# Performance work log

Measured on AMD Instinct MI355X. Metric: run time of the kernel, lower is better.

## Reference

```python
import jax, jax.numpy as jnp
import numpy as np

N, IN_DIM, HID, HEADS, OUT = 4096, 512, 256, 2, 40
LN_EPS = 1e-5


def setup_inputs() -> dict:
    key = jax.random.key(0)
    ks = jax.random.split(key, 12)
    s_in = 1.0 / np.sqrt(IN_DIM)
    s_o = 1.0 / np.sqrt(2 * HID)
    adj = jax.random.randint(ks[0], (HEADS, N, N), 0, 2).astype(jnp.float32)
    h = jax.random.normal(ks[1], (N, IN_DIM), dtype=jnp.float32)
    Wq = jax.random.uniform(ks[2], (HEADS, IN_DIM, HID), minval=-s_in, maxval=s_in)
    bq = jax.random.uniform(ks[3], (HEADS, HID), minval=-s_in, maxval=s_in)
    Wk = jax.random.uniform(ks[4], (HEADS, IN_DIM, HID), minval=-s_in, maxval=s_in)
    bk = jax.random.uniform(ks[5], (HEADS, HID), minval=-s_in, maxval=s_in)
    Wv = jax.random.uniform(ks[6], (HEADS, IN_DIM, HID), minval=-s_in, maxval=s_in)
    bv = jax.random.uniform(ks[7], (HEADS, HID), minval=-s_in, maxval=s_in)
    Wo = jax.random.uniform(ks[8], (2 * HID, IN_DIM), minval=-s_o, maxval=s_o)
    bo = jax.random.uniform(ks[9], (IN_DIM,), minval=-s_o, maxval=s_o)
    gamma = jnp.ones((IN_DIM,), jnp.float32)
    beta = jnp.zeros((IN_DIM,), jnp.float32)
    Wp = jax.random.uniform(ks[10], (IN_DIM, OUT), minval=-s_in, maxval=s_in)
    bp = jax.random.uniform(ks[11], (OUT,), minval=-s_in, maxval=s_in)
    return dict(adj=adj, h=h, Wq=Wq, bq=bq, Wk=Wk, bk=bk, Wv=Wv, bv=bv,
                Wo=Wo, bo=bo, gamma=gamma, beta=beta, Wp=Wp, bp=bp)


def reference(adj, h, Wq, bq, Wk, bk, Wv, bv, Wo, bo, gamma, beta, Wp, bp):
    # Per-head projections, vectorized over the head axis. [H, N, D]
    Q = jnp.einsum('ni,hid->hnd', h, Wq) + bq[:, None, :]
    K = jnp.einsum('ni,hid->hnd', h, Wk) + bk[:, None, :]
    V = jnp.einsum('ni,hid->hnd', h, Wv) + bv[:, None, :]
    # Dense QK^T, elementwise-multiplied (not -inf masked) by per-head adjacency.
    scores = jnp.einsum('hnd,hmd->hnm', Q, K) * adj          # [H, N, N]
    attn = jax.nn.softmax(scores, axis=-1)
    X = jnp.einsum('hnm,hmd->hnd', attn, V)                  # [H, N, D]
    # cat([X0, X1], dim=1) -> [N, H*D]
    X_final = jnp.transpose(X, (1, 0, 2)).reshape(N, HEADS * HID)
    z = X_final @ Wo + bo                                    # [N, IN_DIM]
    mu = jnp.mean(z, axis=-1, keepdims=True)
    var = jnp.var(z, axis=-1, keepdims=True)
    M = (z - mu) * jax.lax.rsqrt(var + LN_EPS) * gamma + beta
    return jax.nn.softmax(M @ Wp + bp, axis=1)               # [N, OUT]
```

## Files before the change

### kernel.cpp

```cpp
#include <hip/hip_runtime.h>
#include <hip/hip_bf16.h>

#define N_TOK 4096
#define D_IN  512
#define D_HID 256
#define N_OUT 40

typedef _Float16 half8 __attribute__((ext_vector_type(8)));
typedef _Float16 half4 __attribute__((ext_vector_type(4)));
typedef float    f32x4 __attribute__((ext_vector_type(4)));

__device__ __forceinline__ void async_copy16(const _Float16* g, _Float16* l) {
  __builtin_amdgcn_global_load_lds(
      (const __attribute__((address_space(1))) unsigned int*)(g),
      (__attribute__((address_space(3))) unsigned int*)(l), 16, 0, 0);
}

__device__ __forceinline__ void transpose_tile(const float* __restrict__ src, int in_ncols,
                                               _Float16* __restrict__ dst, int out_ncols,
                                               int i0, int d0, float* lds )
{
  int tid = threadIdx.x;
  int l15 = tid & 15, l4 = tid >> 4;
#pragma unroll
  for (int p = 0; p < 4; p++) {
    int ii = p * 16 + l4;
    float4 x = *(const float4*)(src + (size_t)(i0 + ii) * in_ncols + d0 + l15 * 4);
    lds[(l15 * 4 + 0) * 65 + ii] = x.x;
    lds[(l15 * 4 + 1) * 65 + ii] = x.y;
    lds[(l15 * 4 + 2) * 65 + ii] = x.z;
    lds[(l15 * 4 + 3) * 65 + ii] = x.w;
  }
  __syncthreads();
  int dd = tid >> 2, chunk = tid & 3;
  half8 o0, o1;
#pragma unroll
  for (int j = 0; j < 8; j++) o0[j] = (_Float16)lds[dd * 65 + chunk * 16 + j];
#pragma unroll
  for (int j = 0; j < 8; j++) o1[j] = (_Float16)lds[dd * 65 + chunk * 16 + 8 + j];
  *(half8*)(dst + (size_t)(d0 + dd) * out_ncols + i0 + chunk * 16) = o0;
  *(half8*)(dst + (size_t)(d0 + dd) * out_ncols + i0 + chunk * 16 + 8) = o1;
}

__global__ void prep_kernel(const float* __restrict__ h, const float* __restrict__ Wq,
                            const float* __restrict__ Wk, const float* __restrict__ Wv,
                            const float* __restrict__ Wo, const float* __restrict__ Wp,
                            _Float16* __restrict__ h16, _Float16* __restrict__ Wqt,
                            _Float16* __restrict__ Wkt, _Float16* __restrict__ Wvt,
                            _Float16* __restrict__ Wot, _Float16* __restrict__ Wpt)
{
  __shared__ float lds[64 * 65];
  int b = blockIdx.x, tid = threadIdx.x;
  if (b < 1024) {
    int base = b * 2048 + tid * 8;
    float4 x0 = *(const float4*)(h + base);
    float4 x1 = *(const float4*)(h + base + 4);
    half8 o;
    o[0]=(_Float16)x0.x; o[1]=(_Float16)x0.y; o[2]=(_Float16)x0.z; o[3]=(_Float16)x0.w;
    o[4]=(_Float16)x1.x; o[5]=(_Float16)x1.y; o[6]=(_Float16)x1.z; o[7]=(_Float16)x1.w;
    *(half8*)(h16 + base) = o;
  } else if (b < 1216) {
    int t = b - 1024;
    int mat = t >> 5;
    int m = mat >> 1, head = mat & 1;
    const float* W = (m==0 ? Wq : (m==1 ? Wk : Wv)) + head * (D_IN * D_HID);
    _Float16* Wt   = (m==0 ? Wqt : (m==1 ? Wkt : Wvt)) + head * (D_IN * D_HID);
    int tt = t & 31;
    int i0 = (tt >> 2) * 64, d0 = (tt & 3) * 64;
    transpose_tile(W, D_HID, Wt, D_IN, i0, d0, lds);
  } else if (b < 1280) {
    int t = b - 1216;
    int i0 = (t >> 3) * 64, d0 = (t & 7) * 64;
    transpose_tile(Wo, D_IN, Wot, D_IN, i0, d0, lds);
  } else {
    int blk = b - 1280;
    int idx = blk * 1024 + tid * 4;
    int j = idx >> 9, i = idx & 511;
    half4 o;
#pragma unroll
    for (int u = 0; u < 4; u++)
      o[u] = (j < N_OUT) ? (_Float16)Wp[(i + u) * N_OUT + j] : (_Float16)0.f;
    *(half4*)(Wpt + j * D_IN + i) = o;
  }
}

__global__ __launch_bounds__(256, 2) void proj_kernel(
    const _Float16* __restrict__ h16,
    const _Float16* __restrict__ Wqt, const _Float16* __restrict__ Wkt,
    const _Float16* __restrict__ Wvt,
    const float* __restrict__ bq, const float* __restrict__ bk,
    const float* __restrict__ bv,
    _Float16* __restrict__ Q16, _Float16* __restrict__ K16,
    _Float16* __restrict__ V16)
{
  int b = blockIdx.x;
  int mh = b >> 7, tile = b & 127;
  int mat = mh >> 1, head = mh & 1;
  const _Float16* Wt = (mat==0 ? Wqt : (mat==1 ? Wkt : Wvt)) + head * (D_IN * D_HID);
  const float* bias  = (mat==0 ? bq  : (mat==1 ? bk  : bv )) + head * D_HID;
  _Float16* Out      = (mat==0 ? Q16 : (mat==1 ? K16 : V16)) + head * (N_TOK * D_HID);
  int tid = threadIdx.x, w = tid >> 6, lane = tid & 63, quad = lane >> 4, cL = lane & 15;
  int row = tile * 32 + (w >> 1) * 16;
  int ch = w & 1;
  const f32x4 z4 = {0.f, 0.f, 0.f, 0.f};
  half8 af[16];
#pragma unroll
  for (int t = 0; t < 16; t++)
    af[t] = *(const half8*)(h16 + (row + cL) * D_IN + t * 32 + quad * 8);
  f32x4 acc[8];
#pragma unroll
  for (int i = 0; i < 8; i++) acc[i] = z4;
#pragma unroll
  for (int t = 0; t < 16; t++) {
    half8 bf[8];
#pragma unroll
    for (int nt = 0; nt < 8; nt++)
      bf[nt] = *(const half8*)(Wt + (ch * 128 + nt * 16 + cL) * D_IN + t * 32 + quad * 8);
#pragma unroll
    for (int nt = 0; nt < 8; nt++)
      acc[nt] = __builtin_amdgcn_mfma_f32_16x16x32_f16(af[t], bf[nt], acc[nt], 0, 0, 0);
  }
#pragma unroll
  for (int nt = 0; nt < 8; nt++) {
    int col = ch * 128 + nt * 16 + cL;
    float bb = bias[col];
#pragma unroll
    for (int reg = 0; reg < 4; reg++)
      Out[(row + quad * 4 + reg) * D_HID + col] = (_Float16)(acc[nt][reg] + bb);
  }
}

__global__ void transv_kernel(const _Float16* __restrict__ V16, _Float16* __restrict__ VT16)
{
  __shared__ __align__(16) _Float16 tile[64 * 72];
  int b = blockIdx.x;
  int head = b >> 8, lb = b & 255;
  int n0 = (lb >> 2) * 64, d0 = (lb & 3) * 64;
  const _Float16* Vh = V16 + head * (N_TOK * D_HID);
  _Float16* VTh = VT16 + head * (N_TOK * D_HID);
  int tid = threadIdx.x;
  int rr = tid >> 2, cg = tid & 3;
  half8 x0 = *(const half8*)(Vh + (n0 + rr) * D_HID + d0 + cg * 16);
  half8 x1 = *(const half8*)(Vh + (n0 + rr) * D_HID + d0 + cg * 16 + 8);
  *(half8*)(tile + rr * 72 + cg * 16) = x0;
  *(half8*)(tile + rr * 72 + cg * 16 + 8) = x1;
  __syncthreads();
  half8 o0, o1;
#pragma unroll
  for (int j = 0; j < 8; j++) {
    o0[j] = tile[(cg * 16 + j) * 72 + rr];
    o1[j] = tile[(cg * 16 + 8 + j) * 72 + rr];
  }
  *(half8*)(VTh + (size_t)(d0 + rr) * N_TOK + n0 + cg * 16) = o0;
  *(half8*)(VTh + (size_t)(d0 + rr) * N_TOK + n0 + cg * 16 + 8) = o1;
}

__global__ __launch_bounds__(256, 2) void attn_kernel(
    const float* __restrict__ adj, const _Float16* __restrict__ Q16,
    const _Float16* __restrict__ K16, const _Float16* __restrict__ VT16,
    _Float16* __restrict__ Opart, float* __restrict__ Mpart, float* __restrict__ Lpart)
{
  __shared__ __align__(16) _Float16 Ktile[64 * 256];
  __shared__ __align__(16) _Float16 VTtile[256 * 64];
  __shared__ __align__(16) _Float16 Pbuf[4 * 16 * 72];

  int b = blockIdx.x;
  int head = (b >> 2) & 1;
  int gs = b & 3;
  int q0 = (b >> 3) * 64;

  int tid = threadIdx.x;
  int w = tid >> 6, lane = tid & 63, quad = lane >> 4, cL = lane & 15;

  const _Float16* Qh = Q16 + head * (N_TOK * D_HID);
  const _Float16* Kh = K16 + head * (N_TOK * D_HID);
  const _Float16* Vh = VT16 + head * (N_TOK * D_HID);
  const float* adjh = adj + (size_t)head * N_TOK * N_TOK;

  int qrow = q0 + w * 16;
  int nstart = gs * 1024;
  const f32x4 z4 = {0.f, 0.f, 0.f, 0.f};

  half8 qf[8];
#pragma unroll
  for (int t = 0; t < 8; t++)
    qf[t] = *(const half8*)(Qh + (qrow + cL) * D_HID + t * 32 + quad * 8);

  f32x4 acc[16];
#pragma unroll
  for (int i = 0; i < 16; i++) acc[i] = z4;
  float m_i[4] = {-1e30f, -1e30f, -1e30f, -1e30f};
  float l_i[4] = {0.f, 0.f, 0.f, 0.f};

  _Float16* pb = Pbuf + w * (16 * 72);

  const float* adjR[4];
#pragma unroll
  for (int reg = 0; reg < 4; reg++)
    adjR[reg] = adjh + (size_t)(qrow + quad * 4 + reg) * N_TOK + nstart + cL;

  int l5 = lane >> 5, l31 = lane & 31;
  int l3 = lane >> 3, l7 = lane & 7;

  for (int it = 0; it < 16; ++it) {
    int n0 = nstart + it * 64;

    __syncthreads();

#pragma unroll
    for (int i = 0; i < 8; i++) {
      int g = w * 8 + i;
      int rK = 2 * g + l5;
      int cK = l31 ^ (rK & 7);
      async_copy16(Kh + (size_t)(n0 + rK) * D_HID + cK * 8, Ktile + g * 512);
      int rV = g * 8 + l3;
      int cV = l7 ^ (rV & 7);
      async_copy16(Vh + (size_t)rV * N_TOK + n0 + cV * 8, VTtile + g * 512);
    }
    float av[4][4];
#pragma unroll
    for (int reg = 0; reg < 4; reg++)
#pragma unroll
      for (int ct = 0; ct < 4; ct++)
        av[reg][ct] = __builtin_nontemporal_load(adjR[reg] + it * 64 + ct * 16);

    __syncthreads();

    f32x4 s[4];
#pragma unroll
    for (int ct = 0; ct < 4; ct++) s[ct] = z4;
#pragma unroll
    for (int t = 0; t < 8; t++) {
#pragma unroll
      for (int ct = 0; ct < 4; ct++) {
        int rK = ct * 16 + cL;
        int ck = (t * 4 + quad) ^ (rK & 7);
        half8 kf = *(const half8*)(Ktile + rK * 256 + ck * 8);
        s[ct] = __builtin_amdgcn_mfma_f32_16x16x32_f16(qf[t], kf, s[ct], 0, 0, 0);
      }
    }

    float alpha[4];
#pragma unroll
    for (int reg = 0; reg < 4; reg++) {
#pragma unroll
      for (int ct = 0; ct < 4; ct++) s[ct][reg] *= av[reg][ct];
      float mx = fmaxf(fmaxf(s[0][reg], s[1][reg]), fmaxf(s[2][reg], s[3][reg]));
#pragma unroll
      for (int msk = 1; msk < 16; msk <<= 1) mx = fmaxf(mx, __shfl_xor(mx, msk, 16));
      float mnew = fmaxf(m_i[reg], mx);
      alpha[reg] = __expf(m_i[reg] - mnew);
      m_i[reg] = mnew;
      float rs = 0.f;
#pragma unroll
      for (int ct = 0; ct < 4; ct++) {
        float p = __expf(s[ct][reg] - mnew);
        s[ct][reg] = p;
        rs += p;
      }
#pragma unroll
      for (int msk = 1; msk < 16; msk <<= 1) rs += __shfl_xor(rs, msk, 16);
      l_i[reg] = l_i[reg] * alpha[reg] + rs;
    }

#pragma unroll
    for (int reg = 0; reg < 4; reg++)
#pragma unroll
      for (int ct = 0; ct < 4; ct++)
        pb[(quad * 4 + reg) * 72 + ct * 16 + cL] = (_Float16)s[ct][reg];

#pragma unroll
    for (int dt = 0; dt < 16; dt++)
#pragma unroll
      for (int reg = 0; reg < 4; reg++)
        acc[dt][reg] *= alpha[reg];

    half8 pf0 = *(const half8*)(pb + cL * 72 + quad * 8);
    half8 pf1 = *(const half8*)(pb + cL * 72 + 32 + quad * 8);
#pragma unroll
    for (int dt = 0; dt < 16; dt++) {
      int rV = dt * 16 + cL;
      int c0 = (quad) ^ (rV & 7);
      int c1 = (4 + quad) ^ (rV & 7);
      half8 v0 = *(const half8*)(VTtile + rV * 64 + c0 * 8);
      half8 v1 = *(const half8*)(VTtile + rV * 64 + c1 * 8);
      acc[dt] = __builtin_amdgcn_mfma_f32_16x16x32_f16(pf0, v0, acc[dt], 0, 0, 0);
      acc[dt] = __builtin_amdgcn_mfma_f32_16x16x32_f16(pf1, v1, acc[dt], 0, 0, 0);
    }
  }

  int prow = (head * 4 + gs) * N_TOK + qrow + quad * 4;
#pragma unroll
  for (int reg = 0; reg < 4; reg++) {
    int row = prow + reg;
#pragma unroll
    for (int dt = 0; dt < 16; dt++)
      Opart[(size_t)row * D_HID + dt * 16 + cL] = (_Float16)acc[dt][reg];
    if (cL == 0) { Mpart[row] = m_i[reg]; Lpart[row] = l_i[reg]; }
  }
}

__global__ void merge_kernel(const _Float16* __restrict__ Opart,
                             const float* __restrict__ Mpart,
                             const float* __restrict__ Lpart,
                             _Float16* __restrict__ Xf)
{
  int t = blockIdx.x * 256 + threadIdx.x;
  int dg = (t & 63) << 2;
  int n = (t >> 6) & (N_TOK - 1);
  int head = t >> 18;
  int idx[4];
  float m[4], l[4];
  float mm = -1e30f;
#pragma unroll
  for (int s = 0; s < 4; s++) {
    idx[s] = (head * 4 + s) * N_TOK + n;
    m[s] = Mpart[idx[s]];
    l[s] = Lpart[idx[s]];
    mm = fmaxf(mm, m[s]);
  }
  float f[4], L = 0.f;
#pragma unroll
  for (int s = 0; s < 4; s++) { f[s] = __expf(m[s] - mm); L += f[s] * l[s]; }
  float rl = 1.0f / L;
  float o[4] = {0.f, 0.f, 0.f, 0.f};
#pragma unroll
  for (int s = 0; s < 4; s++) {
    half4 os = *(const half4*)(Opart + (size_t)idx[s] * D_HID + dg);
#pragma unroll
    for (int u = 0; u < 4; u++) o[u] += (float)os[u] * f[s];
  }
  half4 res;
#pragma unroll
  for (int u = 0; u < 4; u++) res[u] = (_Float16)(o[u] * rl);
  *(half4*)(Xf + (size_t)n * D_IN + head * D_HID + dg) = res;
}

__global__ void final_kernel(
    const _Float16* __restrict__ Xf, const _Float16* __restrict__ Wot,
    const _Float16* __restrict__ Wpt, const float* __restrict__ bo,
    const float* __restrict__ gamma, const float* __restrict__ beta,
    const float* __restrict__ bp, float* __restrict__ out)
{
  __shared__ __align__(16) _Float16 Mlds[16 * 520];
  __shared__ float outs[16 * 48];
  __shared__ float lnsum[4][16], lnsq[4][16];
  __shared__ float smx[16], srl[16];

  int rowbase = blockIdx.x * 16;
  int tid = threadIdx.x, ch = tid >> 6, lane = tid & 63, quad = lane >> 4, cL = lane & 15;
  const f32x4 z4 = {0.f, 0.f, 0.f, 0.f};

  half8 af[16];
#pragma unroll
  for (int t = 0; t < 16; t++)
    af[t] = *(const half8*)(Xf + (rowbase + cL) * D_IN + t * 32 + quad * 8);

  f32x4 acc[8];
#pragma unroll
  for (int i = 0; i < 8; i++) acc[i] = z4;
#pragma unroll
  for (int t = 0; t < 16; t++) {
    half8 bf[8];
#pragma unroll
    for (int nt = 0; nt < 8; nt++)
      bf[nt] = *(const half8*)(Wot + (ch * 128 + nt * 16 + cL) * D_IN + t * 32 + quad * 8);
#pragma unroll
    for (int nt = 0; nt < 8; nt++)
      acc[nt] = __builtin_amdgcn_mfma_f32_16x16x32_f16(af[t], bf[nt], acc[nt], 0, 0, 0);
  }

  float sum[4] = {0, 0, 0, 0}, sq[4] = {0, 0, 0, 0};
#pragma unroll
  for (int nt = 0; nt < 8; nt++) {
    int col = ch * 128 + nt * 16 + cL;
    float bb = bo[col];
#pragma unroll
    for (int reg = 0; reg < 4; reg++) {
      float z = acc[nt][reg] + bb;
      acc[nt][reg] = z;
      sum[reg] += z;
      sq[reg] += z * z;
    }
  }
#pragma unroll
  for (int reg = 0; reg < 4; reg++) {
#pragma unroll
    for (int msk = 1; msk < 16; msk <<= 1) {
      sum[reg] += __shfl_xor(sum[reg], msk, 16);
      sq[reg]  += __shfl_xor(sq[reg], msk, 16);
    }
  }
  if (cL == 0) {
#pragma unroll
    for (int reg = 0; reg < 4; reg++) {
      lnsum[ch][quad * 4 + reg] = sum[reg];
      lnsq[ch][quad * 4 + reg]  = sq[reg];
    }
  }
  __syncthreads();
  float mean[4], rstd[4];
#pragma unroll
  for (int reg = 0; reg < 4; reg++) {
    int row = quad * 4 + reg;
    float s  = lnsum[0][row] + lnsum[1][row] + lnsum[2][row] + lnsum[3][row];
    float s2 = lnsq[0][row]  + lnsq[1][row]  + lnsq[2][row]  + lnsq[3][row];
    float mu = s * (1.0f / 512.0f);
    float var = s2 * (1.0f / 512.0f) - mu * mu;
    mean[reg] = mu;
    rstd[reg] = rsqrtf(var + 1e-5f);
  }
#pragma unroll
  for (int nt = 0; nt < 8; nt++) {
    int col = ch * 128 + nt * 16 + cL;
    float g = gamma[col], be = beta[col];
#pragma unroll
    for (int reg = 0; reg < 4; reg++) {
      float mval = (acc[nt][reg] - mean[reg]) * rstd[reg] * g + be;
      Mlds[(quad * 4 + reg) * 520 + col] = (_Float16)mval;
    }
  }
  __syncthreads();
  if (ch < 3) {
    int jt = ch;
    f32x4 a2 = z4;
#pragma unroll
    for (int t = 0; t < 16; t++) {
      half8 am = *(const half8*)(Mlds + cL * 520 + t * 32 + quad * 8);
      half8 bm = *(const half8*)(Wpt + (jt * 16 + cL) * D_IN + t * 32 + quad * 8);
      a2 = __builtin_amdgcn_mfma_f32_16x16x32_f16(am, bm, a2, 0, 0, 0);
    }
    int col = jt * 16 + cL;
    float bpv = (col < N_OUT) ? bp[col] : 0.0f;
#pragma unroll
    for (int reg = 0; reg < 4; reg++)
      outs[(quad * 4 + reg) * 48 + col] = a2[reg] + bpv;
  }
  __syncthreads();
  if (tid < 16) {
    int row = tid;
    float mx = -1e30f;
    for (int j = 0; j < N_OUT; j++) mx = fmaxf(mx, outs[row * 48 + j]);
    float ssum = 0.f;
    for (int j = 0; j < N_OUT; j++) ssum += __expf(outs[row * 48 + j] - mx);
    smx[row] = mx;
    srl[row] = 1.0f / ssum;
  }
  __syncthreads();
#pragma unroll
  for (int i = 0; i < 3; i++) {
    int lin = tid + 256 * i;
    if (lin < 16 * N_OUT) {
      int row = lin / N_OUT, col = lin % N_OUT;
      out[(size_t)(rowbase + row) * N_OUT + col] =
          __expf(outs[row * 48 + col] - smx[row]) * srl[row];
    }
  }
}

#define OFF_WOT   0u
#define OFF_WPT   524288u
#define OFF_Q16   573440u
#define OFF_K16   4767744u
#define OFF_VT16  8962048u
#define OFF_MP    13156352u
#define OFF_LP    13287424u
#define OFF_XF    13418496u
#define OFF_OP    17612800u
#define OFF_H16   17612800u
#define OFF_WQT   21807104u
#define OFF_WKT   22331392u
#define OFF_WVT   22855680u
#define OFF_V16   23379968u

extern "C" void kernel_launch(void* const* d_in, const int* in_sizes, int n_in,
                              void* d_out, int out_size, void* d_ws, size_t ws_size,
                              hipStream_t stream)
{
  const float* adj   = (const float*)d_in[0];
  const float* h     = (const float*)d_in[1];
  const float* Wq    = (const float*)d_in[2];
  const float* bq    = (const float*)d_in[3];
  const float* Wk    = (const float*)d_in[4];
  const float* bk    = (const float*)d_in[5];
  const float* Wv    = (const float*)d_in[6];
  const float* bv    = (const float*)d_in[7];
  const float* Wo    = (const float*)d_in[8];
  const float* bo    = (const float*)d_in[9];
  const float* gamma = (const float*)d_in[10];
  const float* beta  = (const float*)d_in[11];
  const float* Wp    = (const float*)d_in[12];
  const float* bp    = (const float*)d_in[13];
  float* out = (float*)d_out;
  char* ws = (char*)d_ws;

  _Float16* h16   = (_Float16*)(ws + OFF_H16);
  _Float16* Wqt   = (_Float16*)(ws + OFF_WQT);
  _Float16* Wkt   = (_Float16*)(ws + OFF_WKT);
  _Float16* Wvt   = (_Float16*)(ws + OFF_WVT);
  _Float16* Wot   = (_Float16*)(ws + OFF_WOT);
  _Float16* Wpt   = (_Float16*)(ws + OFF_WPT);
  _Float16* Q16   = (_Float16*)(ws + OFF_Q16);
  _Float16* K16   = (_Float16*)(ws + OFF_K16);
  _Float16* V16   = (_Float16*)(ws + OFF_V16);
  _Float16* VT16  = (_Float16*)(ws + OFF_VT16);
  _Float16* Opart = (_Float16*)(ws + OFF_OP);
  float*    Mpart = (float*)(ws + OFF_MP);
  float*    Lpart = (float*)(ws + OFF_LP);
  _Float16* Xf    = (_Float16*)(ws + OFF_XF);

  prep_kernel<<<1304, 256, 0, stream>>>(h, Wq, Wk, Wv, Wo, Wp,
                                        h16, Wqt, Wkt, Wvt, Wot, Wpt);
  proj_kernel<<<768, 256, 0, stream>>>(h16, Wqt, Wkt, Wvt, bq, bk, bv,
                                       Q16, K16, V16);
  transv_kernel<<<512, 256, 0, stream>>>(V16, VT16);
  attn_kernel<<<512, 256, 0, stream>>>(adj, Q16, K16, VT16, Opart, Mpart, Lpart);
  merge_kernel<<<2048, 256, 0, stream>>>(Opart, Mpart, Lpart, Xf);
  final_kernel<<<256, 256, 0, stream>>>(Xf, Wot, Wpt, bo, gamma, beta, bp, out);
}
```

Baseline: 345.7 us.

## Tile QKV projection through LDS, emit V transposed, stage Wo in LDS

The QKV projection becomes a 128x128 LDS-tiled GEMM fed by async global-to-LDS copies with an XOR swizzle. Q and K come from one concatenated weight, and V is computed as Wv·hᵀ so it is written already transposed, which removes the separate transpose kernel and the V16 round trip. The final kernel now stages Wo chunks in LDS instead of having each wave read weights straight from global memory. The costs are larger LDS use (one block per CU in final_kernel), extra barriers, and strided scalar stores for the transposed V.

Result: faster. 297.9 us (-13.8%).

```diff
diff --git a/kernel.cpp b/kernel.cpp
--- a/kernel.cpp
+++ b/kernel.cpp
@@ -85,74 +85,112 @@
 }
 
 __global__ __launch_bounds__(256, 2) void proj_kernel(
-    const _Float16* __restrict__ h16,
-    const _Float16* __restrict__ Wqt, const _Float16* __restrict__ Wkt,
+    const _Float16* __restrict__ h16, const _Float16* __restrict__ W6 ,
     const _Float16* __restrict__ Wvt,
     const float* __restrict__ bq, const float* __restrict__ bk,
     const float* __restrict__ bv,
     _Float16* __restrict__ Q16, _Float16* __restrict__ K16,
-    _Float16* __restrict__ V16)
-{
+    _Float16* __restrict__ VT16)
+{
+  __shared__ __align__(16) _Float16 Atile[128 * 64];
+  __shared__ __align__(16) _Float16 Btile[128 * 64];
+
   int b = blockIdx.x;
-  int mh = b >> 7, tile = b & 127;
-  int mat = mh >> 1, head = mh & 1;
-  const _Float16* Wt = (mat==0 ? Wqt : (mat==1 ? Wkt : Wvt)) + head * (D_IN * D_HID);
-  const float* bias  = (mat==0 ? bq  : (mat==1 ? bk  : bv )) + head * D_HID;
-  _Float16* Out      = (mat==0 ? Q16 : (mat==1 ? K16 : V16)) + head * (N_TOK * D_HID);
   int tid = threadIdx.x, w = tid >> 6, lane = tid & 63, quad = lane >> 4, cL = lane & 15;
-  int row = tile * 32 + (w >> 1) * 16;
-  int ch = w & 1;
+  int wr = w >> 1, wc = w & 1;
+
+  const _Float16 *Asrc, *Bsrc;
+  int isV;
+  int m0 = 0, n0 = 0, head = 0, mh = 0;
+  if (b < 256) {
+    isV = 0;
+    m0 = (b >> 3) * 128;
+    int ct = b & 7;
+    mh = ct >> 1;
+    n0 = (ct & 1) * 128;
+    Asrc = h16 + (size_t)m0 * D_IN;
+    Bsrc = W6 + (size_t)(ct * 128) * D_IN;
+  } else {
+    isV = 1;
+    int t = b - 256;
+    head = t >> 6;
+    int tt = t & 63;
+    m0 = (tt >> 5) * 128;
+    n0 = (tt & 31) * 128;
+    Asrc = Wvt + (size_t)head * (D_HID * D_IN) + (size_t)m0 * D_IN;
+    Bsrc = h16 + (size_t)n0 * D_IN;
+  }
+
   const f32x4 z4 = {0.f, 0.f, 0.f, 0.f};
-  half8 af[16];
-#pragma unroll
-  for (int t = 0; t < 16; t++)
-    af[t] = *(const half8*)(h16 + (row + cL) * D_IN + t * 32 + quad * 8);
-  f32x4 acc[8];
-#pragma unroll
-  for (int i = 0; i < 8; i++) acc[i] = z4;
-#pragma unroll
-  for (int t = 0; t < 16; t++) {
-    half8 bf[8];
-#pragma unroll
-    for (int nt = 0; nt < 8; nt++)
-      bf[nt] = *(const half8*)(Wt + (ch * 128 + nt * 16 + cL) * D_IN + t * 32 + quad * 8);
-#pragma unroll
-    for (int nt = 0; nt < 8; nt++)
-      acc[nt] = __builtin_amdgcn_mfma_f32_16x16x32_f16(af[t], bf[nt], acc[nt], 0, 0, 0);
-  }
-#pragma unroll
-  for (int nt = 0; nt < 8; nt++) {
-    int col = ch * 128 + nt * 16 + cL;
-    float bb = bias[col];
-#pragma unroll
-    for (int reg = 0; reg < 4; reg++)
-      Out[(row + quad * 4 + reg) * D_HID + col] = (_Float16)(acc[nt][reg] + bb);
-  }
-}
-
-__global__ void transv_kernel(const _Float16* __restrict__ V16, _Float16* __restrict__ VT16)
-{
-  __shared__ __align__(16) _Float16 tile[64 * 72];
-  int b = blockIdx.x;
-  int head = b >> 8, lb = b & 255;
-  int n0 = (lb >> 2) * 64, d0 = (lb & 3) * 64;
-  const _Float16* Vh = V16 + head * (N_TOK * D_HID);
-  _Float16* VTh = VT16 + head * (N_TOK * D_HID);
-  int tid = threadIdx.x;
-  int rr = tid >> 2, cg = tid & 3;
-  half8 x0 = *(const half8*)(Vh + (n0 + rr) * D_HID + d0 + cg * 16);
-  half8 x1 = *(const half8*)(Vh + (n0 + rr) * D_HID + d0 + cg * 16 + 8);
-  *(half8*)(tile + rr * 72 + cg * 16) = x0;
-  *(half8*)(tile + rr * 72 + cg * 16 + 8) = x1;
-  __syncthreads();
-  half8 o0, o1;
-#pragma unroll
-  for (int j = 0; j < 8; j++) {
-    o0[j] = tile[(cg * 16 + j) * 72 + rr];
-    o1[j] = tile[(cg * 16 + 8 + j) * 72 + rr];
-  }
-  *(half8*)(VTh + (size_t)(d0 + rr) * N_TOK + n0 + cg * 16) = o0;
-  *(half8*)(VTh + (size_t)(d0 + rr) * N_TOK + n0 + cg * 16 + 8) = o1;
+  f32x4 acc[4][4];
+#pragma unroll
+  for (int i = 0; i < 4; i++)
+#pragma unroll
+    for (int j = 0; j < 4; j++) acc[i][j] = z4;
+
+  int r8 = lane >> 3, chs = (lane & 7) ^ r8;
+
+  for (int kc = 0; kc < 8; kc++) {
+    __syncthreads();
+#pragma unroll
+    for (int g = 0; g < 4; g++) {
+      int row = (w * 4 + g) * 8 + r8;
+      async_copy16(Asrc + (size_t)row * D_IN + kc * 64 + chs * 8, Atile + (w * 4 + g) * 512);
+      async_copy16(Bsrc + (size_t)row * D_IN + kc * 64 + chs * 8, Btile + (w * 4 + g) * 512);
+    }
+    __syncthreads();
+#pragma unroll
+    for (int kk = 0; kk < 2; kk++) {
+      int ch = ((kk * 4 + quad) ^ (cL & 7)) * 8;
+      half8 a[4], bf[4];
+#pragma unroll
+      for (int mt = 0; mt < 4; mt++)
+        a[mt] = *(const half8*)(Atile + (wr * 64 + mt * 16 + cL) * 64 + ch);
+#pragma unroll
+      for (int nt = 0; nt < 4; nt++)
+        bf[nt] = *(const half8*)(Btile + (wc * 64 + nt * 16 + cL) * 64 + ch);
+#pragma unroll
+      for (int mt = 0; mt < 4; mt++)
+#pragma unroll
+        for (int nt = 0; nt < 4; nt++)
+          acc[mt][nt] = __builtin_amdgcn_mfma_f32_16x16x32_f16(a[mt], bf[nt], acc[mt][nt], 0, 0, 0);
+    }
+  }
+
+  if (!isV) {
+    _Float16* Out = (mh < 2 ? Q16 + (size_t)mh * (N_TOK * D_HID)
+                            : K16 + (size_t)(mh - 2) * (N_TOK * D_HID));
+    const float* bias = (mh < 2 ? bq + mh * D_HID : bk + (mh - 2) * D_HID);
+#pragma unroll
+    for (int mt = 0; mt < 4; mt++) {
+      int row = m0 + wr * 64 + mt * 16 + quad * 4;
+#pragma unroll
+      for (int nt = 0; nt < 4; nt++) {
+        int colg = n0 + wc * 64 + nt * 16 + cL;
+        float bb = bias[colg];
+#pragma unroll
+        for (int reg = 0; reg < 4; reg++)
+          Out[(size_t)(row + reg) * D_HID + colg] = (_Float16)(acc[mt][nt][reg] + bb);
+      }
+    }
+  } else {
+    _Float16* VTh = VT16 + (size_t)head * (N_TOK * D_HID);
+    const float* bvh = bv + head * D_HID;
+#pragma unroll
+    for (int mt = 0; mt < 4; mt++) {
+      int d0r = m0 + wr * 64 + mt * 16 + quad * 4;
+      float bvv[4];
+#pragma unroll
+      for (int reg = 0; reg < 4; reg++) bvv[reg] = bvh[d0r + reg];
+#pragma unroll
+      for (int nt = 0; nt < 4; nt++) {
+        int tok = n0 + wc * 64 + nt * 16 + cL;
+#pragma unroll
+        for (int reg = 0; reg < 4; reg++)
+          VTh[(size_t)(d0r + reg) * N_TOK + tok] = (_Float16)(acc[mt][nt][reg] + bvv[reg]);
+      }
+    }
+  }
 }
 
 __global__ __launch_bounds__(256, 2) void attn_kernel(
@@ -336,19 +374,20 @@
   *(half4*)(Xf + (size_t)n * D_IN + head * D_HID + dg) = res;
 }
 
-__global__ void final_kernel(
+__global__ __launch_bounds__(256, 1) void final_kernel(
     const _Float16* __restrict__ Xf, const _Float16* __restrict__ Wot,
     const _Float16* __restrict__ Wpt, const float* __restrict__ bo,
     const float* __restrict__ gamma, const float* __restrict__ beta,
     const float* __restrict__ bp, float* __restrict__ out)
 {
+  __shared__ __align__(16) _Float16 Btile[512 * 64];
   __shared__ __align__(16) _Float16 Mlds[16 * 520];
   __shared__ float outs[16 * 48];
   __shared__ float lnsum[4][16], lnsq[4][16];
   __shared__ float smx[16], srl[16];
 
   int rowbase = blockIdx.x * 16;
-  int tid = threadIdx.x, ch = tid >> 6, lane = tid & 63, quad = lane >> 4, cL = lane & 15;
+  int tid = threadIdx.x, w = tid >> 6, lane = tid & 63, quad = lane >> 4, cL = lane & 15;
   const f32x4 z4 = {0.f, 0.f, 0.f, 0.f};
 
   half8 af[16];
@@ -359,21 +398,35 @@
   f32x4 acc[8];
 #pragma unroll
   for (int i = 0; i < 8; i++) acc[i] = z4;
-#pragma unroll
-  for (int t = 0; t < 16; t++) {
-    half8 bf[8];
-#pragma unroll
-    for (int nt = 0; nt < 8; nt++)
-      bf[nt] = *(const half8*)(Wot + (ch * 128 + nt * 16 + cL) * D_IN + t * 32 + quad * 8);
-#pragma unroll
-    for (int nt = 0; nt < 8; nt++)
-      acc[nt] = __builtin_amdgcn_mfma_f32_16x16x32_f16(af[t], bf[nt], acc[nt], 0, 0, 0);
+
+  int r8 = lane >> 3, chs = (lane & 7) ^ r8;
+
+  for (int kc = 0; kc < 8; kc++) {
+    __syncthreads();
+#pragma unroll
+    for (int g = 0; g < 16; g++) {
+      int row = (w * 16 + g) * 8 + r8;
+      async_copy16(Wot + (size_t)row * D_IN + kc * 64 + chs * 8, Btile + (w * 16 + g) * 512);
+    }
+    __syncthreads();
+#pragma unroll
+    for (int kk = 0; kk < 2; kk++) {
+      int ch = ((kk * 4 + quad) ^ (cL & 7)) * 8;
+      half8 a = af[kc * 2 + kk];
+      half8 bf[8];
+#pragma unroll
+      for (int nt = 0; nt < 8; nt++)
+        bf[nt] = *(const half8*)(Btile + (w * 128 + nt * 16 + cL) * 64 + ch);
+#pragma unroll
+      for (int nt = 0; nt < 8; nt++)
+        acc[nt] = __builtin_amdgcn_mfma_f32_16x16x32_f16(a, bf[nt], acc[nt], 0, 0, 0);
+    }
   }
 
   float sum[4] = {0, 0, 0, 0}, sq[4] = {0, 0, 0, 0};
 #pragma unroll
   for (int nt = 0; nt < 8; nt++) {
-    int col = ch * 128 + nt * 16 + cL;
+    int col = w * 128 + nt * 16 + cL;
     float bb = bo[col];
 #pragma unroll
     for (int reg = 0; reg < 4; reg++) {
@@ -394,8 +447,8 @@
   if (cL == 0) {
 #pragma unroll
     for (int reg = 0; reg < 4; reg++) {
-      lnsum[ch][quad * 4 + reg] = sum[reg];
-      lnsq[ch][quad * 4 + reg]  = sq[reg];
+      lnsum[w][quad * 4 + reg] = sum[reg];
+      lnsq[w][quad * 4 + reg]  = sq[reg];
     }
   }
   __syncthreads();
@@ -412,7 +465,7 @@
   }
 #pragma unroll
   for (int nt = 0; nt < 8; nt++) {
-    int col = ch * 128 + nt * 16 + cL;
+    int col = w * 128 + nt * 16 + cL;
     float g = gamma[col], be = beta[col];
 #pragma unroll
     for (int reg = 0; reg < 4; reg++) {
@@ -421,8 +474,8 @@
     }
   }
   __syncthreads();
-  if (ch < 3) {
-    int jt = ch;
+  if (w < 3) {
+    int jt = w;
     f32x4 a2 = z4;
 #pragma unroll
     for (int t = 0; t < 16; t++) {
@@ -471,7 +524,6 @@
 #define OFF_WQT   21807104u
 #define OFF_WKT   22331392u
 #define OFF_WVT   22855680u
-#define OFF_V16   23379968u
 
 extern "C" void kernel_launch(void* const* d_in, const int* in_sizes, int n_in,
                               void* d_out, int out_size, void* d_ws, size_t ws_size,
@@ -502,7 +554,6 @@
   _Float16* Wpt   = (_Float16*)(ws + OFF_WPT);
   _Float16* Q16   = (_Float16*)(ws + OFF_Q16);
   _Float16* K16   = (_Float16*)(ws + OFF_K16);
-  _Float16* V16   = (_Float16*)(ws + OFF_V16);
   _Float16* VT16  = (_Float16*)(ws + OFF_VT16);
   _Float16* Opart = (_Float16*)(ws + OFF_OP);
   float*    Mpart = (float*)(ws + OFF_MP);
@@ -511,9 +562,8 @@
 
   prep_kernel<<<1304, 256, 0, stream>>>(h, Wq, Wk, Wv, Wo, Wp,
                                         h16, Wqt, Wkt, Wvt, Wot, Wpt);
-  proj_kernel<<<768, 256, 0, stream>>>(h16, Wqt, Wkt, Wvt, bq, bk, bv,
-                                       Q16, K16, V16);
-  transv_kernel<<<512, 256, 0, stream>>>(V16, VT16);
+  proj_kernel<<<384, 256, 0, stream>>>(h16, Wqt, Wvt, bq, bk, bv,
+                                       Q16, K16, VT16);
   attn_kernel<<<512, 256, 0, stream>>>(adj, Q16, K16, VT16, Opart, Mpart, Lpart);
   merge_kernel<<<2048, 256, 0, stream>>>(Opart, Mpart, Lpart, Xf);
   final_kernel<<<256, 256, 0, stream>>>(Xf, Wot, Wpt, bo, gamma, beta, bp, out);
```
